# Kernel optimization log

Hardware: AMD Instinct MI355X
Metric: run time of the kernel (lower is better)

## Reference

```python
import jax, jax.numpy as jnp
from jax import lax
import numpy as np

NDIM = 256
BATCH = 65536
NROT = NDIM * (NDIM - 1) // 2  # comb(ndim, 2) = 32640


def _givens_mat(rots, ii, jj, ndim):
    """Product G_last @ ... @ G_1 of Givens rotations in combinations order.

    Left-multiplying by G(i, j, theta) only modifies rows i and j, so we apply
    each rotation as a rank-2 row update instead of a full matmul (same math
    as the original `plane_rot_mat @ mat` loop).
    """
    def step(mat, carry):
        i, j, th = carry
        c = jnp.cos(th)
        s = jnp.sin(th)
        ri = mat[i]
        rj = mat[j]
        mat = mat.at[i].set(c * ri - s * rj)
        mat = mat.at[j].set(s * ri + c * rj)
        return mat, None

    mat0 = jnp.eye(ndim, dtype=jnp.complex64)
    mat, _ = lax.scan(step, mat0, (ii, jj, rots))
    return mat


def setup_inputs() -> dict:
    key = jax.random.key(0)
    k1, k2, k3, k4 = jax.random.split(key, 4)
    x = jax.random.normal(k1, (BATCH, NDIM), dtype=jnp.float32)
    rots1 = 0.1 * jax.random.normal(k2, (NROT,), dtype=jnp.float32)
    phases = 0.1 * jax.random.normal(k3, (NDIM,), dtype=jnp.float32)
    rots2 = 0.1 * jax.random.normal(k4, (NROT,), dtype=jnp.float32)
    return {"x": x, "rots1": rots1, "phases": phases, "rots2": rots2}


def reference(x, rots1, phases, rots2):
    ndim = x.shape[1]
    # np.triu_indices(ndim, 1) enumerates (i, j) pairs in the same row-major
    # order as itertools.combinations(range(ndim), 2).
    ii_np, jj_np = np.triu_indices(ndim, k=1)
    ii = jnp.asarray(ii_np, dtype=jnp.int32)
    jj = jnp.asarray(jj_np, dtype=jnp.int32)

    # vector_norm: row-wise L2 normalization
    xn = x / jnp.linalg.norm(x, axis=1, keepdims=True)
    xc = xn.astype(jnp.complex64)

    # rot1: y = x @ M1.T with M1 = G_last @ ... @ G_1
    M1 = _givens_mat(rots1, ii, jj, ndim)
    y = xc @ M1.T

    # phase_transforms: x @ diag(exp(i*phases)) == elementwise phase multiply
    y = y * jnp.exp(1j * phases)

    # rot2
    M2 = _givens_mat(rots2, ii, jj, ndim)
    y = y @ M2.T

    # measure: |.|^2
    return jnp.abs(y) ** 2
```

## Files before the change

### kernel.cpp

```cpp
#include <hip/hip_runtime.h>
#include <stdint.h>
#include <math.h>

#define NDIM 256
#define BATCH 65536
#define NROT 32640

typedef float  f32x4 __attribute__((ext_vector_type(4)));
typedef short  s16x8 __attribute__((ext_vector_type(8)));
typedef unsigned int u32x4 __attribute__((ext_vector_type(4)));
typedef unsigned int u32x2 __attribute__((ext_vector_type(2)));

static __device__ __forceinline__ unsigned short f2bf(float f) {
    unsigned int u = __float_as_uint(f);
    u += 0x7fffu + ((u >> 16) & 1u);
    return (unsigned short)(u >> 16);
}
static __device__ __forceinline__ float bf2f(unsigned short h) {
    return __uint_as_float(((unsigned)h) << 16);
}

static __device__ __forceinline__ void split4(f32x4 v, u32x2* hi, u32x2* lo) {
    unsigned short h[4], l[4];
    #pragma unroll
    for (int i = 0; i < 4; i++) {
        h[i] = f2bf(v[i]);
        l[i] = f2bf(v[i] - bf2f(h[i]));
    }
    *hi = (u32x2){ (unsigned)h[0] | ((unsigned)h[1] << 16),
                   (unsigned)h[2] | ((unsigned)h[3] << 16) };
    *lo = (u32x2){ (unsigned)l[0] | ((unsigned)l[1] << 16),
                   (unsigned)l[2] | ((unsigned)l[3] << 16) };
}
static __device__ __forceinline__ void split8(const float* v, u32x4* hi, u32x4* lo) {
    unsigned short h[8], l[8];
    #pragma unroll
    for (int i = 0; i < 8; i++) {
        h[i] = f2bf(v[i]);
        l[i] = f2bf(v[i] - bf2f(h[i]));
    }
    *hi = (u32x4){ (unsigned)h[0] | ((unsigned)h[1] << 16),
                   (unsigned)h[2] | ((unsigned)h[3] << 16),
                   (unsigned)h[4] | ((unsigned)h[5] << 16),
                   (unsigned)h[6] | ((unsigned)h[7] << 16) };
    *lo = (u32x4){ (unsigned)l[0] | ((unsigned)l[1] << 16),
                   (unsigned)l[2] | ((unsigned)l[3] << 16),
                   (unsigned)l[4] | ((unsigned)l[5] << 16),
                   (unsigned)l[6] | ((unsigned)l[7] << 16) };
}

static __device__ __forceinline__ int sweep_bound(int k, int pblk) {
    int target = k * (NROT / pblk);
    int best = 0, bd = 0x7fffffff;
    for (int i = 0; i <= 256; i += 4) {
        int pre = i * 255 - (i * (i - 1)) / 2;
        int d = pre - target; d = (d < 0) ? -d : d;
        if (d < bd) { bd = d; best = i; }
    }
    return best;
}

__global__ __launch_bounds__(256) void k_cs(const float* __restrict__ r1,
                                            const float* __restrict__ r2,
                                            float2* __restrict__ cs) {
    int i = blockIdx.x * 256 + threadIdx.x;
    float th = (i < NROT) ? r1[i] : r2[i - NROT];
    float sv, cv; sincosf(th, &sv, &cv);
    cs[i] = make_float2(cv, sv);
}

__global__ __launch_bounds__(64) void k_blocks(const float2* __restrict__ cs,
                                               float* __restrict__ bmats, int pblk) {
    __shared__ float colb[264 * 64];
    __shared__ float2 csb[2][256 * 4];
    __shared__ float2 tri[24 * 6];

    const int t = threadIdx.x;
    const int bid = blockIdx.x;
    const int chunk = bid & 3;
    const int b = (bid >> 2) % pblk;
    const int set = (bid >> 2) / pblk;
    const int col0 = chunk * 64;
    const float2* cst = cs + (size_t)set * NROT;

    const int s0 = sweep_bound(b, pblk);
    const int s1 = sweep_bound(b + 1, pblk);
    const int ngroups = (s1 - s0) >> 2;

    {
        const f32x4 z = {0.f, 0.f, 0.f, 0.f};
        #pragma unroll 11
        for (int q = 0; q < 66; q++)
            *(f32x4*)&colb[(q * 64 + t) * 4] = z;
        colb[(col0 + t) * 64 + t] = 1.0f;
    }

    for (int k = t; k < ngroups * 6; k += 64) {
        int g = k / 6, q = k - g * 6;
        int a  = (q < 3) ? 0 : ((q < 5) ? 1 : 2);
        int bb = (q < 3) ? (q + 1) : ((q < 5) ? (q - 1) : 3);
        int m0 = s0 + g * 4;
        int m = m0 + a;
        int base = m * 255 - (m * (m - 1)) / 2;
        tri[k] = cst[base - m - 1 + m0 + bb];
    }

    float2 gv[16];
    {
        const int m0g = s0;
        int offg[4];
        #pragma unroll
        for (int a = 0; a < 4; a++) {
            int m = m0g + a;
            offg[a] = m * 255 - (m * (m - 1)) / 2 - m - 1;
        }
        #pragma unroll
        for (int it = 0; it < 16; it++) {
            int k = t + it * 64;
            int jj = k >> 2, a = k & 3;
            int j = m0g + 4 + jj;
            gv[it] = (j < 256) ? cst[offg[a] + j] : make_float2(1.f, 0.f);
        }
        #pragma unroll
        for (int it = 0; it < 16; it++)
            csb[0][t + it * 64] = gv[it];
    }

    for (int g = 0; g < ngroups; g++) {
        const int m0 = s0 + g * 4;
        const int buf = g & 1;
        const int n_j = 252 - m0;
        const int n_p = (n_j > 0) ? ((n_j + 7) & ~7) : 0;
        const float* csbuf = (const float*)&csb[buf][0];

        const bool have_next = (g + 1 < ngroups);
        if (have_next) {
            const int m0g = m0 + 4;
            int offg[4];
            #pragma unroll
            for (int a = 0; a < 4; a++) {
                int m = m0g + a;
                offg[a] = m * 255 - (m * (m - 1)) / 2 - m - 1;
            }
            #pragma unroll
            for (int it = 0; it < 16; it++) {
                int k = t + it * 64;
                int jj = k >> 2, a = k & 3;
                int j = m0g + 4 + jj;
                gv[it] = (j < 256) ? cst[offg[a] + j] : make_float2(1.f, 0.f);
            }
        }

        float u0 = colb[(m0 + 0) * 64 + t];
        float u1 = colb[(m0 + 1) * 64 + t];
        float u2 = colb[(m0 + 2) * 64 + t];
        float u3 = colb[(m0 + 3) * 64 + t];

        {
            float2 cv; float nr;
            cv = tri[g * 6 + 0]; nr = cv.y * u0 + cv.x * u1; u0 = cv.x * u0 - cv.y * u1; u1 = nr;
            cv = tri[g * 6 + 1]; nr = cv.y * u0 + cv.x * u2; u0 = cv.x * u0 - cv.y * u2; u2 = nr;
            cv = tri[g * 6 + 2]; nr = cv.y * u0 + cv.x * u3; u0 = cv.x * u0 - cv.y * u3; u3 = nr;
            cv = tri[g * 6 + 3]; nr = cv.y * u1 + cv.x * u2; u1 = cv.x * u1 - cv.y * u2; u2 = nr;
            cv = tri[g * 6 + 4]; nr = cv.y * u1 + cv.x * u3; u1 = cv.x * u1 - cv.y * u3; u3 = nr;
            cv = tri[g * 6 + 5]; nr = cv.y * u2 + cv.x * u3; u2 = cv.x * u2 - cv.y * u3; u3 = nr;
        }

        if (n_p > 0) {
            float rbuf[8];
            f32x4 abuf[8][2];
            #pragma unroll
            for (int p = 0; p < 8; p++) {
                rbuf[p] = colb[(m0 + 4 + p) * 64 + t];
                abuf[p][0] = *(const f32x4*)&csbuf[p * 8 + 0];
                abuf[p][1] = *(const f32x4*)&csbuf[p * 8 + 4];
            }
            for (int c = 0; c < n_p; c += 8) {
                #pragma unroll
                for (int p = 0; p < 8; p++) {
                    const int j = m0 + 4 + c + p;
                    float r = rbuf[p];
                    f32x4 A01 = abuf[p][0], A23 = abuf[p][1];
                    int jn = j + 8; jn = (jn < 263) ? jn : 263;
                    int cn = c + p + 8; cn = (cn < n_p) ? cn : (n_p - 1);
                    rbuf[p] = colb[jn * 64 + t];
                    abuf[p][0] = *(const f32x4*)&csbuf[cn * 8 + 0];
                    abuf[p][1] = *(const f32x4*)&csbuf[cn * 8 + 4];
                    float nr;
                    nr = A01[1] * u0 + A01[0] * r; u0 = A01[0] * u0 - A01[1] * r; r = nr;
                    nr = A01[3] * u1 + A01[2] * r; u1 = A01[2] * u1 - A01[3] * r; r = nr;
                    nr = A23[1] * u2 + A23[0] * r; u2 = A23[0] * u2 - A23[1] * r; r = nr;
                    nr = A23[3] * u3 + A23[2] * r; u3 = A23[2] * u3 - A23[3] * r; r = nr;
                    colb[j * 64 + t] = r;
                }
            }
        }
        colb[(m0 + 0) * 64 + t] = u0;
        colb[(m0 + 1) * 64 + t] = u1;
        colb[(m0 + 2) * 64 + t] = u2;
        colb[(m0 + 3) * 64 + t] = u3;

        if (have_next) {
            #pragma unroll
            for (int it = 0; it < 16; it++)
                csb[buf ^ 1][t + it * 64] = gv[it];
        }
    }

    float* outm = bmats + (size_t)(set * pblk + b) * 65536;
    for (int r = 0; r < 256; r++)
        outm[(size_t)r * 256 + col0 + t] = colb[r * 64 + t];
}

__global__ __launch_bounds__(256) void k_combine(const float* __restrict__ src,
                                                 float* __restrict__ dst,
                                                 int half, int pblk,
                                                 const float* __restrict__ xg,
                                                 unsigned short* __restrict__ xbf) {
    const int by = blockIdx.y;
    const int tid = threadIdx.x;

    if (by >= 2 * half) {
        const int id = (by - 2 * half) * 16 + blockIdx.x;
        const int w = tid >> 6, lane = tid & 63;
        const int r0 = id * 64;
        #pragma unroll 2
        for (int p = 0; p < 16; p++) {
            int row = r0 + p * 4 + w;
            f32x4 v = *(const f32x4*)&xg[(size_t)row * 256 + lane * 4];
            float s = v[0] * v[0] + v[1] * v[1] + v[2] * v[2] + v[3] * v[3];
            #pragma unroll
            for (int off = 32; off; off >>= 1) s += __shfl_xor(s, off, 64);
            float sc = 1.0f / sqrtf(s);
            unsigned short h0 = f2bf(v[0] * sc), h1 = f2bf(v[1] * sc);
            unsigned short h2 = f2bf(v[2] * sc), h3 = f2bf(v[3] * sc);
            u32x2 pk = { (unsigned)h0 | ((unsigned)h1 << 16),
                         (unsigned)h2 | ((unsigned)h3 << 16) };
            *(u32x2*)&xbf[(size_t)row * 256 + lane * 4] = pk;
        }
        return;
    }

    const int set = by / half, pidx = by % half;
    const int stride = pblk / (2 * half);
    const int s0A = sweep_bound((2 * pidx + 1) * stride, pblk);
    const float* Am = src + (size_t)(set * 2 * half + 2 * pidx + 1) * 65536;
    const float* Bm = src + (size_t)(set * 2 * half + 2 * pidx) * 65536;
    float* Dm = dst + (size_t)(set * half + pidx) * 65536;
    const int tr = blockIdx.x >> 2, tc = blockIdx.x & 3;

    if (tr * 64 + 64 <= s0A) {
        #pragma unroll
        for (int it = 0; it < 4; it++) {
            int flat = tid + it * 256;
            int r = flat >> 4, c4 = flat & 15;
            size_t idx = (size_t)(tr * 64 + r) * 256 + tc * 64 + c4 * 4;
            *(f32x4*)&Dm[idx] = *(const f32x4*)&Bm[idx];
        }
        return;
    }
    const int kb0 = (tr * 64 >= s0A) ? (s0A >> 5) : 0;

    __shared__ unsigned short Ahi[64 * 40], Alo[64 * 40];
    __shared__ unsigned short Bhi[64 * 40], Blo[64 * 40];

    const int lane = tid & 63, w = tid >> 6;
    const int mh = (w >> 1) * 32, nh = (w & 1) * 32;
    const int l15 = lane & 15, lq = lane >> 4;
    const int bn = tid & 63, bkq = tid >> 6;

    f32x4 acc[2][2];
    #pragma unroll
    for (int i = 0; i < 2; i++)
        #pragma unroll
        for (int j = 0; j < 2; j++) acc[i][j] = (f32x4){0.f, 0.f, 0.f, 0.f};

    for (int kb = kb0; kb < 8; kb++) {
        __syncthreads();
        #pragma unroll
        for (int it = 0; it < 2; it++) {
            int flat = tid + it * 256;
            int r = flat >> 3, c4 = flat & 7;
            f32x4 v = *(const f32x4*)&Am[(size_t)(tr * 64 + r) * 256 + kb * 32 + c4 * 4];
            u32x2 hi, lo; split4(v, &hi, &lo);
            *(u32x2*)&Ahi[r * 40 + c4 * 4] = hi;
            *(u32x2*)&Alo[r * 40 + c4 * 4] = lo;
        }
        {
            float bv[8];
            #pragma unroll
            for (int i = 0; i < 8; i++)
                bv[i] = Bm[(size_t)(kb * 32 + bkq * 8 + i) * 256 + tc * 64 + bn];
            u32x4 hi, lo; split8(bv, &hi, &lo);
            *(u32x4*)&Bhi[bn * 40 + bkq * 8] = hi;
            *(u32x4*)&Blo[bn * 40 + bkq * 8] = lo;
        }
        __syncthreads();
        s16x8 ah[2], al[2], bh[2], bl[2];
        #pragma unroll
        for (int tm = 0; tm < 2; tm++) {
            ah[tm] = *(const s16x8*)&Ahi[(mh + tm * 16 + l15) * 40 + lq * 8];
            al[tm] = *(const s16x8*)&Alo[(mh + tm * 16 + l15) * 40 + lq * 8];
        }
        #pragma unroll
        for (int tn = 0; tn < 2; tn++) {
            bh[tn] = *(const s16x8*)&Bhi[(nh + tn * 16 + l15) * 40 + lq * 8];
            bl[tn] = *(const s16x8*)&Blo[(nh + tn * 16 + l15) * 40 + lq * 8];
        }
        #pragma unroll
        for (int tm = 0; tm < 2; tm++)
            #pragma unroll
            for (int tn = 0; tn < 2; tn++) {
                acc[tm][tn] = __builtin_amdgcn_mfma_f32_16x16x32_bf16(ah[tm], bh[tn], acc[tm][tn], 0, 0, 0);
                acc[tm][tn] = __builtin_amdgcn_mfma_f32_16x16x32_bf16(ah[tm], bl[tn], acc[tm][tn], 0, 0, 0);
                acc[tm][tn] = __builtin_amdgcn_mfma_f32_16x16x32_bf16(al[tm], bh[tn], acc[tm][tn], 0, 0, 0);
            }
    }
    #pragma unroll
    for (int tm = 0; tm < 2; tm++)
        #pragma unroll
        for (int tn = 0; tn < 2; tn++)
            #pragma unroll
            for (int r = 0; r < 4; r++)
                Dm[(size_t)(tr * 64 + mh + tm * 16 + lq * 4 + r) * 256
                   + tc * 64 + nh + tn * 16 + l15] = acc[tm][tn][r];
}

__global__ __launch_bounds__(256) void k_abt(const float* __restrict__ mats,
                                             const float* __restrict__ phases,
                                             unsigned short* __restrict__ abt) {
    const float* Am = mats + 65536;
    const float* Bm = mats;
    const int v = blockIdx.y;
    const int tr = blockIdx.x >> 2, tc = blockIdx.x & 3;
    const int tid = threadIdx.x;

    __shared__ unsigned short Ahi[64 * 40], Alo[64 * 40];
    __shared__ unsigned short Bhi[64 * 40], Blo[64 * 40];

    const int lane = tid & 63, w = tid >> 6;
    const int mh = (w >> 1) * 32, nh = (w & 1) * 32;
    const int l15 = lane & 15, lq = lane >> 4;
    const int bn = tid & 63, bkq = tid >> 6;

    f32x4 acc[2][2];
    #pragma unroll
    for (int i = 0; i < 2; i++)
        #pragma unroll
        for (int j = 0; j < 2; j++) acc[i][j] = (f32x4){0.f, 0.f, 0.f, 0.f};

    for (int kb = 0; kb < 8; kb++) {
        __syncthreads();
        #pragma unroll
        for (int it = 0; it < 2; it++) {
            int flat = tid + it * 256;
            int r = flat >> 3, c4 = flat & 7;
            f32x4 vv = *(const f32x4*)&Am[(size_t)(tr * 64 + r) * 256 + kb * 32 + c4 * 4];
            u32x2 hi, lo; split4(vv, &hi, &lo);
            *(u32x2*)&Ahi[r * 40 + c4 * 4] = hi;
            *(u32x2*)&Alo[r * 40 + c4 * 4] = lo;
        }
        {
            float bv[8];
            #pragma unroll
            for (int i = 0; i < 8; i++) {
                int kg = kb * 32 + bkq * 8 + i;
                float ph = phases[kg];
                float sc = v ? sinf(ph) : cosf(ph);
                bv[i] = Bm[(size_t)kg * 256 + tc * 64 + bn] * sc;
            }
            u32x4 hi, lo; split8(bv, &hi, &lo);
            *(u32x4*)&Bhi[bn * 40 + bkq * 8] = hi;
            *(u32x4*)&Blo[bn * 40 + bkq * 8] = lo;
        }
        __syncthreads();
        s16x8 ah[2], al[2], bh[2], bl[2];
        #pragma unroll
        for (int tm = 0; tm < 2; tm++) {
            ah[tm] = *(const s16x8*)&Ahi[(mh + tm * 16 + l15) * 40 + lq * 8];
            al[tm] = *(const s16x8*)&Alo[(mh + tm * 16 + l15) * 40 + lq * 8];
        }
        #pragma unroll
        for (int tn = 0; tn < 2; tn++) {
            bh[tn] = *(const s16x8*)&Bhi[(nh + tn * 16 + l15) * 40 + lq * 8];
            bl[tn] = *(const s16x8*)&Blo[(nh + tn * 16 + l15) * 40 + lq * 8];
        }
        #pragma unroll
        for (int tm = 0; tm < 2; tm++)
            #pragma unroll
            for (int tn = 0; tn < 2; tn++) {
                acc[tm][tn] = __builtin_amdgcn_mfma_f32_16x16x32_bf16(ah[tm], bh[tn], acc[tm][tn], 0, 0, 0);
                acc[tm][tn] = __builtin_amdgcn_mfma_f32_16x16x32_bf16(ah[tm], bl[tn], acc[tm][tn], 0, 0, 0);
                acc[tm][tn] = __builtin_amdgcn_mfma_f32_16x16x32_bf16(al[tm], bh[tn], acc[tm][tn], 0, 0, 0);
            }
    }
    #pragma unroll
    for (int tm = 0; tm < 2; tm++)
        #pragma unroll
        for (int tn = 0; tn < 2; tn++)
            #pragma unroll
            for (int r = 0; r < 4; r++)
                abt[(size_t)(v * 256 + tr * 64 + mh + tm * 16 + lq * 4 + r) * 256
                    + tc * 64 + nh + tn * 16 + l15] = f2bf(acc[tm][tn][r]);
}

__global__ __launch_bounds__(256) void k_norm(const float* __restrict__ x,
                                              float* __restrict__ invn) {
    const int row = blockIdx.x * 4 + (threadIdx.x >> 6);
    const int lane = threadIdx.x & 63;
    f32x4 v = *(const f32x4*)&x[(size_t)row * 256 + lane * 4];
    float s = v[0] * v[0] + v[1] * v[1] + v[2] * v[2] + v[3] * v[3];
    for (int off = 32; off; off >>= 1) s += __shfl_xor(s, off, 64);
    if (lane == 0) invn[row] = 1.0f / sqrtf(s);
}

#define BKP 136
__global__ __launch_bounds__(256) void k_gemm_bf(const unsigned short* __restrict__ xbf,
                                                 const unsigned short* __restrict__ abt,
                                                 float* __restrict__ out) {
    __shared__ unsigned short As[128 * BKP];
    __shared__ unsigned short Bs[128 * BKP];
    const int tid = threadIdx.x;
    const int l  = blockIdx.y * 4 + blockIdx.x;
    const int L  = (l & 7) * 256 + (l >> 3);
    const int cb = L & 3;
    const int rb = L >> 2;
    const int lane = tid & 63, w = tid >> 6;

    f32x4 acc[16];
    #pragma unroll
    for (int i = 0; i < 16; i++) acc[i] = (f32x4){0.f, 0.f, 0.f, 0.f};

    int rA[8], cA[8], grB[8];
    #pragma unroll
    for (int it = 0; it < 8; it++) {
        int flat = tid + it * 256;
        rA[it] = flat >> 4; cA[it] = flat & 15;
        int r = rA[it];
        grB[it] = (r < 64) ? (cb * 64 + r) : (256 + cb * 64 + (r - 64));
    }

    u32x4 pa[8], pb[8];
    #pragma unroll
    for (int it = 0; it < 8; it++) {
        pa[it] = *(const u32x4*)&xbf[(size_t)(rb * 128 + rA[it]) * 256 + cA[it] * 8];
        pb[it] = *(const u32x4*)&abt[(size_t)grB[it] * 256 + cA[it] * 8];
    }
    #pragma unroll
    for (int it = 0; it < 8; it++) {
        *(u32x4*)&As[rA[it] * BKP + cA[it] * 8] = pa[it];
        *(u32x4*)&Bs[rA[it] * BKP + cA[it] * 8] = pb[it];
    }
    __syncthreads();
    #pragma unroll
    for (int it = 0; it < 8; it++) {
        pa[it] = *(const u32x4*)&xbf[(size_t)(rb * 128 + rA[it]) * 256 + 128 + cA[it] * 8];
        pb[it] = *(const u32x4*)&abt[(size_t)grB[it] * 256 + 128 + cA[it] * 8];
    }

    auto compute = [&]() {
        #pragma unroll
        for (int ks = 0; ks < 4; ks++) {
            const int k0 = ks * 32 + (lane >> 4) * 8;
            s16x8 a[2], b[8];
            #pragma unroll
            for (int tm = 0; tm < 2; tm++)
                a[tm] = *(const s16x8*)&As[(w * 32 + tm * 16 + (lane & 15)) * BKP + k0];
            #pragma unroll
            for (int tn = 0; tn < 8; tn++)
                b[tn] = *(const s16x8*)&Bs[(tn * 16 + (lane & 15)) * BKP + k0];
            #pragma unroll
            for (int tm = 0; tm < 2; tm++)
                #pragma unroll
                for (int tn = 0; tn < 8; tn++)
                    acc[tm * 8 + tn] = __builtin_amdgcn_mfma_f32_16x16x32_bf16(
                        a[tm], b[tn], acc[tm * 8 + tn], 0, 0, 0);
        }
    };
    compute();
    __syncthreads();
    #pragma unroll
    for (int it = 0; it < 8; it++) {
        *(u32x4*)&As[rA[it] * BKP + cA[it] * 8] = pa[it];
        *(u32x4*)&Bs[rA[it] * BKP + cA[it] * 8] = pb[it];
    }
    __syncthreads();
    compute();

    const int qr = lane >> 4, c = lane & 15;
    #pragma unroll
    for (int tm = 0; tm < 2; tm++) {
        #pragma unroll
        for (int tn = 0; tn < 4; tn++) {
            f32x4 p = acc[tm * 8 + tn];
            f32x4 q = acc[tm * 8 + tn + 4];
            #pragma unroll
            for (int r = 0; r < 4; r++) {
                int m = w * 32 + tm * 16 + qr * 4 + r;
                out[(size_t)(rb * 128 + m) * 256 + cb * 64 + tn * 16 + c] =
                    p[r] * p[r] + q[r] * q[r];
            }
        }
    }
}

__global__ __launch_bounds__(256) void k_gemm_f32(const float* __restrict__ x,
                                                  const unsigned short* __restrict__ abt,
                                                  const float* __restrict__ invn,
                                                  float* __restrict__ out) {
    __shared__ unsigned short As[128 * BKP];
    __shared__ unsigned short Bs[128 * BKP];
    const int tid = threadIdx.x;
    const int l  = blockIdx.y * 4 + blockIdx.x;
    const int L  = (l & 7) * 256 + (l >> 3);
    const int cb = L & 3;
    const int rb = L >> 2;
    const int lane = tid & 63, w = tid >> 6;

    f32x4 acc[16];
    #pragma unroll
    for (int i = 0; i < 16; i++) acc[i] = (f32x4){0.f, 0.f, 0.f, 0.f};

    for (int kb = 0; kb < 2; kb++) {
        __syncthreads();
        #pragma unroll
        for (int it = 0; it < 16; it++) {
            int flat = tid + it * 256;
            int r = flat >> 5, c4 = flat & 31;
            f32x4 v = *(const f32x4*)&x[(size_t)(rb * 128 + r) * 256 + kb * 128 + c4 * 4];
            float sc = invn[rb * 128 + r];
            v[0] *= sc; v[1] *= sc; v[2] *= sc; v[3] *= sc;
            unsigned short h0 = f2bf(v[0]), h1 = f2bf(v[1]);
            unsigned short h2 = f2bf(v[2]), h3 = f2bf(v[3]);
            u32x2 pk = { (unsigned)h0 | ((unsigned)h1 << 16),
                         (unsigned)h2 | ((unsigned)h3 << 16) };
            *(u32x2*)&As[r * BKP + c4 * 4] = pk;
        }
        #pragma unroll
        for (int it = 0; it < 8; it++) {
            int flat = tid + it * 256;
            int r = flat >> 4, c8 = flat & 15;
            int gr = (r < 64) ? (cb * 64 + r) : (256 + cb * 64 + (r - 64));
            u32x4 vv = *(const u32x4*)&abt[(size_t)gr * 256 + kb * 128 + c8 * 8];
            *(u32x4*)&Bs[r * BKP + c8 * 8] = vv;
        }
        __syncthreads();
        #pragma unroll
        for (int ks = 0; ks < 4; ks++) {
            const int k0 = ks * 32 + (lane >> 4) * 8;
            s16x8 a[2], b[8];
            #pragma unroll
            for (int tm = 0; tm < 2; tm++)
                a[tm] = *(const s16x8*)&As[(w * 32 + tm * 16 + (lane & 15)) * BKP + k0];
            #pragma unroll
            for (int tn = 0; tn < 8; tn++)
                b[tn] = *(const s16x8*)&Bs[(tn * 16 + (lane & 15)) * BKP + k0];
            #pragma unroll
            for (int tm = 0; tm < 2; tm++)
                #pragma unroll
                for (int tn = 0; tn < 8; tn++)
                    acc[tm * 8 + tn] = __builtin_amdgcn_mfma_f32_16x16x32_bf16(
                        a[tm], b[tn], acc[tm * 8 + tn], 0, 0, 0);
        }
    }

    const int qr = lane >> 4, c = lane & 15;
    #pragma unroll
    for (int tm = 0; tm < 2; tm++) {
        #pragma unroll
        for (int tn = 0; tn < 4; tn++) {
            f32x4 p = acc[tm * 8 + tn];
            f32x4 q = acc[tm * 8 + tn + 4];
            #pragma unroll
            for (int r = 0; r < 4; r++) {
                int m = w * 32 + tm * 16 + qr * 4 + r;
                out[(size_t)(rb * 128 + m) * 256 + cb * 64 + tn * 16 + c] =
                    p[r] * p[r] + q[r] * q[r];
            }
        }
    }
}

extern "C" void kernel_launch(void* const* d_in, const int* in_sizes, int n_in,
                              void* d_out, int out_size, void* d_ws, size_t ws_size,
                              hipStream_t stream) {
    (void)in_sizes; (void)n_in; (void)out_size;
    const float* x      = (const float*)d_in[0];
    const float* rots1  = (const float*)d_in[1];
    const float* phases = (const float*)d_in[2];
    const float* rots2  = (const float*)d_in[3];
    float* out = (float*)d_out;
    char* ws = (char*)d_ws;

    const size_t MAT = 262144;
    int pblk = 32;
    while (pblk > 16 &&
           (size_t)3 * pblk * MAT + 2 * MAT + (size_t)BATCH * 512 > ws_size)
        pblk >>= 1;
    const size_t offA   = 0;
    const size_t offB   = offA + (size_t)2 * pblk * MAT;
    const size_t offABT = offB + (size_t)pblk * MAT;
    const size_t offINV = offABT + MAT;
    const size_t offXBF = offINV + MAT;
    const bool use_xbf = (offXBF + (size_t)BATCH * 512) <= ws_size;

    float*          A    = (float*)(ws + offA);
    float*          B    = (float*)(ws + offB);
    unsigned short* abt  = (unsigned short*)(ws + offABT);
    float*          invn = (float*)(ws + offINV);
    unsigned short* xbf  = (unsigned short*)(ws + offXBF);
    float2*         cs   = (float2*)(ws + offB);

    k_cs<<<(2 * NROT) / 256, 256, 0, stream>>>(rots1, rots2, cs);
    k_blocks<<<8 * pblk, 64, 0, stream>>>(cs, A, pblk);

    float* srcp = A; float* dstp = B;
    bool first = true;
    for (int half = pblk / 2; half >= 1; half >>= 1) {
        const int xny = (first && use_xbf) ? 64 : 0;
        k_combine<<<dim3(16, 2 * half + xny), 256, 0, stream>>>(srcp, dstp, half, pblk,
                                                                x, xbf);
        float* tmp = srcp; srcp = dstp; dstp = tmp;
        first = false;
    }
    k_abt<<<dim3(16, 2), 256, 0, stream>>>(srcp, phases, abt);

    if (use_xbf) {
        k_gemm_bf<<<dim3(4, BATCH / 128), 256, 0, stream>>>(xbf, abt, out);
    } else {
        k_norm<<<BATCH / 4, 256, 0, stream>>>(x, invn);
        k_gemm_f32<<<dim3(4, BATCH / 128), 256, 0, stream>>>(x, abt, invn, out);
    }
}
```

Before: 263.4 us.

## Fuse combine tree and abt into one cooperative kernel; inline sincos into k_blocks

Replaces the sequence of per-level k_combine launches plus k_abt with a single cooperative persistent kernel that uses grid-wide syncs between tree levels, and folds the x normalisation work into the first level. It also removes the separate k_cs kernel by computing sincos directly inside k_blocks. This aims to cut kernel launch gaps and tail idle time across the many small launches. The costs are grid.sync overhead, redundant sincos evaluation across the column-chunk blocks, and reliance on cooperative launch support, with the old path kept as a fallback.

```diff
diff --git a/kernel.cpp b/kernel.cpp
--- a/kernel.cpp
+++ b/kernel.cpp
@@ -1,4 +1,5 @@
 #include <hip/hip_runtime.h>
+#include <hip/hip_cooperative_groups.h>
 #include <stdint.h>
 #include <math.h>
 
@@ -60,16 +61,8 @@
     return best;
 }
 
-__global__ __launch_bounds__(256) void k_cs(const float* __restrict__ r1,
-                                            const float* __restrict__ r2,
-                                            float2* __restrict__ cs) {
-    int i = blockIdx.x * 256 + threadIdx.x;
-    float th = (i < NROT) ? r1[i] : r2[i - NROT];
-    float sv, cv; sincosf(th, &sv, &cv);
-    cs[i] = make_float2(cv, sv);
-}
-
-__global__ __launch_bounds__(64) void k_blocks(const float2* __restrict__ cs,
+__global__ __launch_bounds__(64) void k_blocks(const float* __restrict__ r1,
+                                               const float* __restrict__ r2,
                                                float* __restrict__ bmats, int pblk) {
     __shared__ float colb[264 * 64];
     __shared__ float2 csb[2][256 * 4];
@@ -81,7 +74,7 @@
     const int b = (bid >> 2) % pblk;
     const int set = (bid >> 2) / pblk;
     const int col0 = chunk * 64;
-    const float2* cst = cs + (size_t)set * NROT;
+    const float* rots = set ? r2 : r1;
 
     const int s0 = sweep_bound(b, pblk);
     const int s1 = sweep_bound(b + 1, pblk);
@@ -102,7 +95,9 @@
         int m0 = s0 + g * 4;
         int m = m0 + a;
         int base = m * 255 - (m * (m - 1)) / 2;
-        tri[k] = cst[base - m - 1 + m0 + bb];
+        float th = rots[base - m - 1 + m0 + bb];
+        float sv, cv; sincosf(th, &sv, &cv);
+        tri[k] = make_float2(cv, sv);
     }
 
     float2 gv[16];
@@ -119,7 +114,10 @@
             int k = t + it * 64;
             int jj = k >> 2, a = k & 3;
             int j = m0g + 4 + jj;
-            gv[it] = (j < 256) ? cst[offg[a] + j] : make_float2(1.f, 0.f);
+            if (j < 256) {
+                float sv, cv; sincosf(rots[offg[a] + j], &sv, &cv);
+                gv[it] = make_float2(cv, sv);
+            } else gv[it] = make_float2(1.f, 0.f);
         }
         #pragma unroll
         for (int it = 0; it < 16; it++)
@@ -147,7 +145,10 @@
                 int k = t + it * 64;
                 int jj = k >> 2, a = k & 3;
                 int j = m0g + 4 + jj;
-                gv[it] = (j < 256) ? cst[offg[a] + j] : make_float2(1.f, 0.f);
+                if (j < 256) {
+                    float sv, cv; sincosf(rots[offg[a] + j], &sv, &cv);
+                    gv[it] = make_float2(cv, sv);
+                } else gv[it] = make_float2(1.f, 0.f);
             }
         }
 
@@ -212,42 +213,40 @@
         outm[(size_t)r * 256 + col0 + t] = colb[r * 64 + t];
 }
 
-__global__ __launch_bounds__(256) void k_combine(const float* __restrict__ src,
-                                                 float* __restrict__ dst,
-                                                 int half, int pblk,
-                                                 const float* __restrict__ xg,
-                                                 unsigned short* __restrict__ xbf) {
-    const int by = blockIdx.y;
-    const int tid = threadIdx.x;
-
-    if (by >= 2 * half) {
-        const int id = (by - 2 * half) * 16 + blockIdx.x;
-        const int w = tid >> 6, lane = tid & 63;
-        const int r0 = id * 64;
-        #pragma unroll 2
-        for (int p = 0; p < 16; p++) {
-            int row = r0 + p * 4 + w;
-            f32x4 v = *(const f32x4*)&xg[(size_t)row * 256 + lane * 4];
-            float s = v[0] * v[0] + v[1] * v[1] + v[2] * v[2] + v[3] * v[3];
-            #pragma unroll
-            for (int off = 32; off; off >>= 1) s += __shfl_xor(s, off, 64);
-            float sc = 1.0f / sqrtf(s);
-            unsigned short h0 = f2bf(v[0] * sc), h1 = f2bf(v[1] * sc);
-            unsigned short h2 = f2bf(v[2] * sc), h3 = f2bf(v[3] * sc);
-            u32x2 pk = { (unsigned)h0 | ((unsigned)h1 << 16),
-                         (unsigned)h2 | ((unsigned)h3 << 16) };
-            *(u32x2*)&xbf[(size_t)row * 256 + lane * 4] = pk;
-        }
-        return;
-    }
-
+
+static __device__ __forceinline__ void xnorm_item(const float* __restrict__ xg,
+                                                  unsigned short* __restrict__ xbf,
+                                                  int id, int tid) {
+    const int w = tid >> 6, lane = tid & 63;
+    const int r0 = id * 64;
+    #pragma unroll 2
+    for (int p = 0; p < 16; p++) {
+        int row = r0 + p * 4 + w;
+        f32x4 v = *(const f32x4*)&xg[(size_t)row * 256 + lane * 4];
+        float s = v[0] * v[0] + v[1] * v[1] + v[2] * v[2] + v[3] * v[3];
+        #pragma unroll
+        for (int off = 32; off; off >>= 1) s += __shfl_xor(s, off, 64);
+        float sc = 1.0f / sqrtf(s);
+        unsigned short h0 = f2bf(v[0] * sc), h1 = f2bf(v[1] * sc);
+        unsigned short h2 = f2bf(v[2] * sc), h3 = f2bf(v[3] * sc);
+        u32x2 pk = { (unsigned)h0 | ((unsigned)h1 << 16),
+                     (unsigned)h2 | ((unsigned)h3 << 16) };
+        *(u32x2*)&xbf[(size_t)row * 256 + lane * 4] = pk;
+    }
+}
+
+static __device__ void combine_tile(const float* __restrict__ src,
+                                    float* __restrict__ dst,
+                                    int half, int pblk, int bx, int by, int tid,
+                                    unsigned short* Ahi, unsigned short* Alo,
+                                    unsigned short* Bhi, unsigned short* Blo) {
     const int set = by / half, pidx = by % half;
     const int stride = pblk / (2 * half);
     const int s0A = sweep_bound((2 * pidx + 1) * stride, pblk);
     const float* Am = src + (size_t)(set * 2 * half + 2 * pidx + 1) * 65536;
     const float* Bm = src + (size_t)(set * 2 * half + 2 * pidx) * 65536;
     float* Dm = dst + (size_t)(set * half + pidx) * 65536;
-    const int tr = blockIdx.x >> 2, tc = blockIdx.x & 3;
+    const int tr = bx >> 2, tc = bx & 3;
 
     if (tr * 64 + 64 <= s0A) {
         #pragma unroll
@@ -260,9 +259,6 @@
         return;
     }
     const int kb0 = (tr * 64 >= s0A) ? (s0A >> 5) : 0;
-
-    __shared__ unsigned short Ahi[64 * 40], Alo[64 * 40];
-    __shared__ unsigned short Bhi[64 * 40], Blo[64 * 40];
 
     const int lane = tid & 63, w = tid >> 6;
     const int mh = (w >> 1) * 32, nh = (w & 1) * 32;
@@ -326,17 +322,15 @@
                    + tc * 64 + nh + tn * 16 + l15] = acc[tm][tn][r];
 }
 
-__global__ __launch_bounds__(256) void k_abt(const float* __restrict__ mats,
-                                             const float* __restrict__ phases,
-                                             unsigned short* __restrict__ abt) {
+static __device__ void abt_tile(const float* __restrict__ mats,
+                                const float* __restrict__ phases,
+                                unsigned short* __restrict__ abtp,
+                                int bx, int v, int tid,
+                                unsigned short* Ahi, unsigned short* Alo,
+                                unsigned short* Bhi, unsigned short* Blo) {
     const float* Am = mats + 65536;
     const float* Bm = mats;
-    const int v = blockIdx.y;
-    const int tr = blockIdx.x >> 2, tc = blockIdx.x & 3;
-    const int tid = threadIdx.x;
-
-    __shared__ unsigned short Ahi[64 * 40], Alo[64 * 40];
-    __shared__ unsigned short Bhi[64 * 40], Blo[64 * 40];
+    const int tr = bx >> 2, tc = bx & 3;
 
     const int lane = tid & 63, w = tid >> 6;
     const int mh = (w >> 1) * 32, nh = (w & 1) * 32;
@@ -400,8 +394,66 @@
         for (int tn = 0; tn < 2; tn++)
             #pragma unroll
             for (int r = 0; r < 4; r++)
-                abt[(size_t)(v * 256 + tr * 64 + mh + tm * 16 + lq * 4 + r) * 256
-                    + tc * 64 + nh + tn * 16 + l15] = f2bf(acc[tm][tn][r]);
+                abtp[(size_t)(v * 256 + tr * 64 + mh + tm * 16 + lq * 4 + r) * 256
+                     + tc * 64 + nh + tn * 16 + l15] = f2bf(acc[tm][tn][r]);
+}
+
+__global__ __launch_bounds__(256) void k_tree(const float* __restrict__ A0,
+                                              float* __restrict__ B0,
+                                              int pblk,
+                                              const float* __restrict__ phases,
+                                              unsigned short* __restrict__ abtp,
+                                              const float* __restrict__ xg,
+                                              unsigned short* __restrict__ xbf,
+                                              int do_xn) {
+    __shared__ unsigned short Ahi[64 * 40], Alo[64 * 40];
+    __shared__ unsigned short Bhi[64 * 40], Blo[64 * 40];
+    cooperative_groups::grid_group grid = cooperative_groups::this_grid();
+    const int GW = gridDim.x;
+    const int tid = threadIdx.x;
+    const float* srcp = A0;
+    float* dstp = B0;
+    int first = 1;
+    for (int half = pblk / 2; half >= 1; half >>= 1) {
+        const int ctiles = 16 * 2 * half;
+        const int items = ctiles + ((first && do_xn) ? 1024 : 0);
+        for (int it = blockIdx.x; it < items; it += GW) {
+            if (it < ctiles)
+                combine_tile(srcp, dstp, half, pblk, it & 15, it >> 4, tid,
+                             Ahi, Alo, Bhi, Blo);
+            else
+                xnorm_item(xg, xbf, it - ctiles, tid);
+        }
+        grid.sync();
+        const float* ts = srcp; srcp = dstp; dstp = (float*)ts;
+        first = 0;
+    }
+    for (int it = blockIdx.x; it < 32; it += GW)
+        abt_tile(srcp, phases, abtp, it & 15, it >> 4, tid, Ahi, Alo, Bhi, Blo);
+}
+
+__global__ __launch_bounds__(256) void k_combine(const float* __restrict__ src,
+                                                 float* __restrict__ dst,
+                                                 int half, int pblk,
+                                                 const float* __restrict__ xg,
+                                                 unsigned short* __restrict__ xbf) {
+    __shared__ unsigned short Ahi[64 * 40], Alo[64 * 40];
+    __shared__ unsigned short Bhi[64 * 40], Blo[64 * 40];
+    const int by = blockIdx.y, tid = threadIdx.x;
+    if (by >= 2 * half) {
+        xnorm_item(xg, xbf, (by - 2 * half) * 16 + blockIdx.x, tid);
+        return;
+    }
+    combine_tile(src, dst, half, pblk, blockIdx.x, by, tid, Ahi, Alo, Bhi, Blo);
+}
+
+__global__ __launch_bounds__(256) void k_abt(const float* __restrict__ mats,
+                                             const float* __restrict__ phases,
+                                             unsigned short* __restrict__ abtp) {
+    __shared__ unsigned short Ahi[64 * 40], Alo[64 * 40];
+    __shared__ unsigned short Bhi[64 * 40], Blo[64 * 40];
+    abt_tile(mats, phases, abtp, blockIdx.x, blockIdx.y, threadIdx.x,
+             Ahi, Alo, Bhi, Blo);
 }
 
 __global__ __launch_bounds__(256) void k_norm(const float* __restrict__ x,
@@ -609,21 +661,35 @@
     unsigned short* abt  = (unsigned short*)(ws + offABT);
     float*          invn = (float*)(ws + offINV);
     unsigned short* xbf  = (unsigned short*)(ws + offXBF);
-    float2*         cs   = (float2*)(ws + offB);
-
-    k_cs<<<(2 * NROT) / 256, 256, 0, stream>>>(rots1, rots2, cs);
-    k_blocks<<<8 * pblk, 64, 0, stream>>>(cs, A, pblk);
-
-    float* srcp = A; float* dstp = B;
-    bool first = true;
-    for (int half = pblk / 2; half >= 1; half >>= 1) {
-        const int xny = (first && use_xbf) ? 64 : 0;
-        k_combine<<<dim3(16, 2 * half + xny), 256, 0, stream>>>(srcp, dstp, half, pblk,
-                                                                x, xbf);
-        float* tmp = srcp; srcp = dstp; dstp = tmp;
-        first = false;
-    }
-    k_abt<<<dim3(16, 2), 256, 0, stream>>>(srcp, phases, abt);
+
+    k_blocks<<<8 * pblk, 64, 0, stream>>>(rots1, rots2, A, pblk);
+
+    bool coop_ok = false;
+    if (use_xbf) {
+        int maxb = 0;
+        if (hipOccupancyMaxActiveBlocksPerMultiprocessor(&maxb, k_tree, 256, 0)
+                == hipSuccess && maxb >= 1) {
+            int gw = maxb * 256; if (gw > 1024) gw = 1024;
+            int do_xn = 1;
+            void* kargs[] = { (void*)&A, (void*)&B, (void*)&pblk, (void*)&phases,
+                              (void*)&abt, (void*)&x, (void*)&xbf, (void*)&do_xn };
+            if (hipLaunchCooperativeKernel((void*)k_tree, dim3(gw), dim3(256),
+                                           kargs, 0, stream) == hipSuccess)
+                coop_ok = true;
+        }
+    }
+    if (!coop_ok) {
+        float* srcp = A; float* dstp = B;
+        bool first = true;
+        for (int half = pblk / 2; half >= 1; half >>= 1) {
+            const int xny = (first && use_xbf) ? 64 : 0;
+            k_combine<<<dim3(16, 2 * half + xny), 256, 0, stream>>>(srcp, dstp, half,
+                                                                    pblk, x, xbf);
+            float* tmp = srcp; srcp = dstp; dstp = tmp;
+            first = false;
+        }
+        k_abt<<<dim3(16, 2), 256, 0, stream>>>(srcp, phases, abt);
+    }
 
     if (use_xbf) {
         k_gemm_bf<<<dim3(4, BATCH / 128), 256, 0, stream>>>(xbf, abt, out);
```

New measurement: 438.1 us. +66.3%, slower.

## Double-buffer shared tiles and prefetch two k-steps ahead in combine and abt kernels

Applied to the files above, without the earlier changes.

Restructures the split-bf16 MFMA tile loops in k_combine and k_abt into a register-prefetched, double-buffered LDS pipeline. Global loads for tile k+2 are issued while tile k+1 is split into shared memory and tile k is multiplied, which leaves one barrier per step instead of two. The aim is to hide global-load latency in these small, latency-bound matrix-combine kernels. In exchange it doubles LDS use per block (about 40 KB) and raises register pressure, which could lower occupancy. The final large GEMM is unchanged.

```diff
diff --git a/kernel.cpp b/kernel.cpp
--- a/kernel.cpp
+++ b/kernel.cpp
@@ -212,42 +212,103 @@
         outm[(size_t)r * 256 + col0 + t] = colb[r * 64 + t];
 }
 
-__global__ __launch_bounds__(256) void k_combine(const float* __restrict__ src,
-                                                 float* __restrict__ dst,
-                                                 int half, int pblk,
-                                                 const float* __restrict__ xg,
-                                                 unsigned short* __restrict__ xbf) {
-    const int by = blockIdx.y;
-    const int tid = threadIdx.x;
-
-    if (by >= 2 * half) {
-        const int id = (by - 2 * half) * 16 + blockIdx.x;
-        const int w = tid >> 6, lane = tid & 63;
-        const int r0 = id * 64;
-        #pragma unroll 2
-        for (int p = 0; p < 16; p++) {
-            int row = r0 + p * 4 + w;
-            f32x4 v = *(const f32x4*)&xg[(size_t)row * 256 + lane * 4];
-            float s = v[0] * v[0] + v[1] * v[1] + v[2] * v[2] + v[3] * v[3];
-            #pragma unroll
-            for (int off = 32; off; off >>= 1) s += __shfl_xor(s, off, 64);
-            float sc = 1.0f / sqrtf(s);
-            unsigned short h0 = f2bf(v[0] * sc), h1 = f2bf(v[1] * sc);
-            unsigned short h2 = f2bf(v[2] * sc), h3 = f2bf(v[3] * sc);
-            u32x2 pk = { (unsigned)h0 | ((unsigned)h1 << 16),
-                         (unsigned)h2 | ((unsigned)h3 << 16) };
-            *(u32x2*)&xbf[(size_t)row * 256 + lane * 4] = pk;
-        }
-        return;
-    }
-
+static __device__ __forceinline__ void xnorm_item(const float* __restrict__ xg,
+                                                  unsigned short* __restrict__ xbf,
+                                                  int id, int tid) {
+    const int w = tid >> 6, lane = tid & 63;
+    const int r0 = id * 64;
+    #pragma unroll 2
+    for (int p = 0; p < 16; p++) {
+        int row = r0 + p * 4 + w;
+        f32x4 v = *(const f32x4*)&xg[(size_t)row * 256 + lane * 4];
+        float s = v[0] * v[0] + v[1] * v[1] + v[2] * v[2] + v[3] * v[3];
+        #pragma unroll
+        for (int off = 32; off; off >>= 1) s += __shfl_xor(s, off, 64);
+        float sc = 1.0f / sqrtf(s);
+        unsigned short h0 = f2bf(v[0] * sc), h1 = f2bf(v[1] * sc);
+        unsigned short h2 = f2bf(v[2] * sc), h3 = f2bf(v[3] * sc);
+        u32x2 pk = { (unsigned)h0 | ((unsigned)h1 << 16),
+                     (unsigned)h2 | ((unsigned)h3 << 16) };
+        *(u32x2*)&xbf[(size_t)row * 256 + lane * 4] = pk;
+    }
+}
+
+#define TB 2560
+
+static __device__ __forceinline__ void tile_issueA(const float* __restrict__ Am,
+                                                   int tr, int kb, int tid,
+                                                   f32x4 va[2]) {
+    #pragma unroll
+    for (int it = 0; it < 2; it++) {
+        int flat = tid + it * 256;
+        int r = flat >> 3, c4 = flat & 7;
+        va[it] = *(const f32x4*)&Am[(size_t)(tr * 64 + r) * 256 + kb * 32 + c4 * 4];
+    }
+}
+static __device__ __forceinline__ void tile_issueB(const float* __restrict__ Bm,
+                                                   int tc, int kb, int bn, int bkq,
+                                                   float vb[8]) {
+    #pragma unroll
+    for (int i = 0; i < 8; i++)
+        vb[i] = Bm[(size_t)(kb * 32 + bkq * 8 + i) * 256 + tc * 64 + bn];
+}
+static __device__ __forceinline__ void tile_commit(unsigned short* __restrict__ Ahi,
+                                                   unsigned short* __restrict__ Alo,
+                                                   unsigned short* __restrict__ Bhi,
+                                                   unsigned short* __restrict__ Blo,
+                                                   int tid, int bn, int bkq,
+                                                   const f32x4 va[2], const float vb[8]) {
+    #pragma unroll
+    for (int it = 0; it < 2; it++) {
+        int flat = tid + it * 256;
+        int r = flat >> 3, c4 = flat & 7;
+        u32x2 hi, lo; split4(va[it], &hi, &lo);
+        *(u32x2*)&Ahi[r * 40 + c4 * 4] = hi;
+        *(u32x2*)&Alo[r * 40 + c4 * 4] = lo;
+    }
+    u32x4 hi8, lo8; split8(vb, &hi8, &lo8);
+    *(u32x4*)&Bhi[bn * 40 + bkq * 8] = hi8;
+    *(u32x4*)&Blo[bn * 40 + bkq * 8] = lo8;
+}
+static __device__ __forceinline__ void tile_mfma(const unsigned short* __restrict__ Ahi,
+                                                 const unsigned short* __restrict__ Alo,
+                                                 const unsigned short* __restrict__ Bhi,
+                                                 const unsigned short* __restrict__ Blo,
+                                                 int mh, int nh, int l15, int lq,
+                                                 f32x4 acc[2][2]) {
+    s16x8 ah[2], al[2], bh[2], bl[2];
+    #pragma unroll
+    for (int tm = 0; tm < 2; tm++) {
+        ah[tm] = *(const s16x8*)&Ahi[(mh + tm * 16 + l15) * 40 + lq * 8];
+        al[tm] = *(const s16x8*)&Alo[(mh + tm * 16 + l15) * 40 + lq * 8];
+    }
+    #pragma unroll
+    for (int tn = 0; tn < 2; tn++) {
+        bh[tn] = *(const s16x8*)&Bhi[(nh + tn * 16 + l15) * 40 + lq * 8];
+        bl[tn] = *(const s16x8*)&Blo[(nh + tn * 16 + l15) * 40 + lq * 8];
+    }
+    #pragma unroll
+    for (int tm = 0; tm < 2; tm++)
+        #pragma unroll
+        for (int tn = 0; tn < 2; tn++) {
+            acc[tm][tn] = __builtin_amdgcn_mfma_f32_16x16x32_bf16(ah[tm], bh[tn], acc[tm][tn], 0, 0, 0);
+            acc[tm][tn] = __builtin_amdgcn_mfma_f32_16x16x32_bf16(ah[tm], bl[tn], acc[tm][tn], 0, 0, 0);
+            acc[tm][tn] = __builtin_amdgcn_mfma_f32_16x16x32_bf16(al[tm], bh[tn], acc[tm][tn], 0, 0, 0);
+        }
+}
+
+static __device__ void combine_tile(const float* __restrict__ src,
+                                    float* __restrict__ dst,
+                                    int half, int pblk, int bx, int by, int tid,
+                                    unsigned short* Ahi, unsigned short* Alo,
+                                    unsigned short* Bhi, unsigned short* Blo) {
     const int set = by / half, pidx = by % half;
     const int stride = pblk / (2 * half);
     const int s0A = sweep_bound((2 * pidx + 1) * stride, pblk);
     const float* Am = src + (size_t)(set * 2 * half + 2 * pidx + 1) * 65536;
     const float* Bm = src + (size_t)(set * 2 * half + 2 * pidx) * 65536;
     float* Dm = dst + (size_t)(set * half + pidx) * 65536;
-    const int tr = blockIdx.x >> 2, tc = blockIdx.x & 3;
+    const int tr = bx >> 2, tc = bx & 3;
 
     if (tr * 64 + 64 <= s0A) {
         #pragma unroll
@@ -261,9 +322,6 @@
     }
     const int kb0 = (tr * 64 >= s0A) ? (s0A >> 5) : 0;
 
-    __shared__ unsigned short Ahi[64 * 40], Alo[64 * 40];
-    __shared__ unsigned short Bhi[64 * 40], Blo[64 * 40];
-
     const int lane = tid & 63, w = tid >> 6;
     const int mh = (w >> 1) * 32, nh = (w & 1) * 32;
     const int l15 = lane & 15, lq = lane >> 4;
@@ -275,46 +333,37 @@
         #pragma unroll
         for (int j = 0; j < 2; j++) acc[i][j] = (f32x4){0.f, 0.f, 0.f, 0.f};
 
+    f32x4 vaE[2], vaO[2]; float vbE[8], vbO[8];
+    tile_issueA(Am, tr, kb0, tid, vaE);
+    tile_issueB(Bm, tc, kb0, bn, bkq, vbE);
+    if (kb0 + 1 < 8) {
+        tile_issueA(Am, tr, kb0 + 1, tid, vaO);
+        tile_issueB(Bm, tc, kb0 + 1, bn, bkq, vbO);
+    }
+    tile_commit(Ahi, Alo, Bhi, Blo, tid, bn, bkq, vaE, vbE);
+    __syncthreads();
+
     for (int kb = kb0; kb < 8; kb++) {
+        const int cur = (kb - kb0) & 1;
+        if (cur == 0) {
+            if (kb + 2 < 8) {
+                tile_issueA(Am, tr, kb + 2, tid, vaE);
+                tile_issueB(Bm, tc, kb + 2, bn, bkq, vbE);
+            }
+            if (kb + 1 < 8)
+                tile_commit(Ahi + TB, Alo + TB, Bhi + TB, Blo + TB,
+                            tid, bn, bkq, vaO, vbO);
+            tile_mfma(Ahi, Alo, Bhi, Blo, mh, nh, l15, lq, acc);
+        } else {
+            if (kb + 2 < 8) {
+                tile_issueA(Am, tr, kb + 2, tid, vaO);
+                tile_issueB(Bm, tc, kb + 2, bn, bkq, vbO);
+            }
+            if (kb + 1 < 8)
+                tile_commit(Ahi, Alo, Bhi, Blo, tid, bn, bkq, vaE, vbE);
+            tile_mfma(Ahi + TB, Alo + TB, Bhi + TB, Blo + TB, mh, nh, l15, lq, acc);
+        }
         __syncthreads();
-        #pragma unroll
-        for (int it = 0; it < 2; it++) {
-            int flat = tid + it * 256;
-            int r = flat >> 3, c4 = flat & 7;
-            f32x4 v = *(const f32x4*)&Am[(size_t)(tr * 64 + r) * 256 + kb * 32 + c4 * 4];
-            u32x2 hi, lo; split4(v, &hi, &lo);
-            *(u32x2*)&Ahi[r * 40 + c4 * 4] = hi;
-            *(u32x2*)&Alo[r * 40 + c4 * 4] = lo;
-        }
-        {
-            float bv[8];
-            #pragma unroll
-            for (int i = 0; i < 8; i++)
-                bv[i] = Bm[(size_t)(kb * 32 + bkq * 8 + i) * 256 + tc * 64 + bn];
-            u32x4 hi, lo; split8(bv, &hi, &lo);
-            *(u32x4*)&Bhi[bn * 40 + bkq * 8] = hi;
-            *(u32x4*)&Blo[bn * 40 + bkq * 8] = lo;
-        }
-        __syncthreads();
-        s16x8 ah[2], al[2], bh[2], bl[2];
-        #pragma unroll
-        for (int tm = 0; tm < 2; tm++) {
-            ah[tm] = *(const s16x8*)&Ahi[(mh + tm * 16 + l15) * 40 + lq * 8];
-            al[tm] = *(const s16x8*)&Alo[(mh + tm * 16 + l15) * 40 + lq * 8];
-        }
-        #pragma unroll
-        for (int tn = 0; tn < 2; tn++) {
-            bh[tn] = *(const s16x8*)&Bhi[(nh + tn * 16 + l15) * 40 + lq * 8];
-            bl[tn] = *(const s16x8*)&Blo[(nh + tn * 16 + l15) * 40 + lq * 8];
-        }
-        #pragma unroll
-        for (int tm = 0; tm < 2; tm++)
-            #pragma unroll
-            for (int tn = 0; tn < 2; tn++) {
-                acc[tm][tn] = __builtin_amdgcn_mfma_f32_16x16x32_bf16(ah[tm], bh[tn], acc[tm][tn], 0, 0, 0);
-                acc[tm][tn] = __builtin_amdgcn_mfma_f32_16x16x32_bf16(ah[tm], bl[tn], acc[tm][tn], 0, 0, 0);
-                acc[tm][tn] = __builtin_amdgcn_mfma_f32_16x16x32_bf16(al[tm], bh[tn], acc[tm][tn], 0, 0, 0);
-            }
     }
     #pragma unroll
     for (int tm = 0; tm < 2; tm++)
@@ -326,17 +375,15 @@
                    + tc * 64 + nh + tn * 16 + l15] = acc[tm][tn][r];
 }
 
-__global__ __launch_bounds__(256) void k_abt(const float* __restrict__ mats,
-                                             const float* __restrict__ phases,
-                                             unsigned short* __restrict__ abt) {
+static __device__ void abt_tile(const float* __restrict__ mats,
+                                const float* __restrict__ phases,
+                                unsigned short* __restrict__ abtp,
+                                int bx, int v, int tid,
+                                unsigned short* Ahi, unsigned short* Alo,
+                                unsigned short* Bhi, unsigned short* Blo) {
     const float* Am = mats + 65536;
     const float* Bm = mats;
-    const int v = blockIdx.y;
-    const int tr = blockIdx.x >> 2, tc = blockIdx.x & 3;
-    const int tid = threadIdx.x;
-
-    __shared__ unsigned short Ahi[64 * 40], Alo[64 * 40];
-    __shared__ unsigned short Bhi[64 * 40], Blo[64 * 40];
+    const int tr = bx >> 2, tc = bx & 3;
 
     const int lane = tid & 63, w = tid >> 6;
     const int mh = (w >> 1) * 32, nh = (w & 1) * 32;
@@ -349,50 +396,37 @@
         #pragma unroll
         for (int j = 0; j < 2; j++) acc[i][j] = (f32x4){0.f, 0.f, 0.f, 0.f};
 
+    auto issueBs = [&](int kb, float vb[8]) {
+        #pragma unroll
+        for (int i = 0; i < 8; i++) {
+            int kg = kb * 32 + bkq * 8 + i;
+            float ph = phases[kg];
+            float sc = v ? sinf(ph) : cosf(ph);
+            vb[i] = Bm[(size_t)kg * 256 + tc * 64 + bn] * sc;
+        }
+    };
+
+    f32x4 vaE[2], vaO[2]; float vbE[8], vbO[8];
+    tile_issueA(Am, tr, 0, tid, vaE); issueBs(0, vbE);
+    tile_issueA(Am, tr, 1, tid, vaO); issueBs(1, vbO);
+    tile_commit(Ahi, Alo, Bhi, Blo, tid, bn, bkq, vaE, vbE);
+    __syncthreads();
+
     for (int kb = 0; kb < 8; kb++) {
+        const int cur = kb & 1;
+        if (cur == 0) {
+            if (kb + 2 < 8) { tile_issueA(Am, tr, kb + 2, tid, vaE); issueBs(kb + 2, vbE); }
+            if (kb + 1 < 8)
+                tile_commit(Ahi + TB, Alo + TB, Bhi + TB, Blo + TB,
+                            tid, bn, bkq, vaO, vbO);
+            tile_mfma(Ahi, Alo, Bhi, Blo, mh, nh, l15, lq, acc);
+        } else {
+            if (kb + 2 < 8) { tile_issueA(Am, tr, kb + 2, tid, vaO); issueBs(kb + 2, vbO); }
+            if (kb + 1 < 8)
+                tile_commit(Ahi, Alo, Bhi, Blo, tid, bn, bkq, vaE, vbE);
+            tile_mfma(Ahi + TB, Alo + TB, Bhi + TB, Blo + TB, mh, nh, l15, lq, acc);
+        }
         __syncthreads();
-        #pragma unroll
-        for (int it = 0; it < 2; it++) {
-            int flat = tid + it * 256;
-            int r = flat >> 3, c4 = flat & 7;
-            f32x4 vv = *(const f32x4*)&Am[(size_t)(tr * 64 + r) * 256 + kb * 32 + c4 * 4];
-            u32x2 hi, lo; split4(vv, &hi, &lo);
-            *(u32x2*)&Ahi[r * 40 + c4 * 4] = hi;
-            *(u32x2*)&Alo[r * 40 + c4 * 4] = lo;
-        }
-        {
-            float bv[8];
-            #pragma unroll
-            for (int i = 0; i < 8; i++) {
-                int kg = kb * 32 + bkq * 8 + i;
-                float ph = phases[kg];
-                float sc = v ? sinf(ph) : cosf(ph);
-                bv[i] = Bm[(size_t)kg * 256 + tc * 64 + bn] * sc;
-            }
-            u32x4 hi, lo; split8(bv, &hi, &lo);
-            *(u32x4*)&Bhi[bn * 40 + bkq * 8] = hi;
-            *(u32x4*)&Blo[bn * 40 + bkq * 8] = lo;
-        }
-        __syncthreads();
-        s16x8 ah[2], al[2], bh[2], bl[2];
-        #pragma unroll
-        for (int tm = 0; tm < 2; tm++) {
-            ah[tm] = *(const s16x8*)&Ahi[(mh + tm * 16 + l15) * 40 + lq * 8];
-            al[tm] = *(const s16x8*)&Alo[(mh + tm * 16 + l15) * 40 + lq * 8];
-        }
-        #pragma unroll
-        for (int tn = 0; tn < 2; tn++) {
-            bh[tn] = *(const s16x8*)&Bhi[(nh + tn * 16 + l15) * 40 + lq * 8];
-            bl[tn] = *(const s16x8*)&Blo[(nh + tn * 16 + l15) * 40 + lq * 8];
-        }
-        #pragma unroll
-        for (int tm = 0; tm < 2; tm++)
-            #pragma unroll
-            for (int tn = 0; tn < 2; tn++) {
-                acc[tm][tn] = __builtin_amdgcn_mfma_f32_16x16x32_bf16(ah[tm], bh[tn], acc[tm][tn], 0, 0, 0);
-                acc[tm][tn] = __builtin_amdgcn_mfma_f32_16x16x32_bf16(ah[tm], bl[tn], acc[tm][tn], 0, 0, 0);
-                acc[tm][tn] = __builtin_amdgcn_mfma_f32_16x16x32_bf16(al[tm], bh[tn], acc[tm][tn], 0, 0, 0);
-            }
     }
     #pragma unroll
     for (int tm = 0; tm < 2; tm++)
@@ -400,8 +434,30 @@
         for (int tn = 0; tn < 2; tn++)
             #pragma unroll
             for (int r = 0; r < 4; r++)
-                abt[(size_t)(v * 256 + tr * 64 + mh + tm * 16 + lq * 4 + r) * 256
-                    + tc * 64 + nh + tn * 16 + l15] = f2bf(acc[tm][tn][r]);
+                abtp[(size_t)(v * 256 + tr * 64 + mh + tm * 16 + lq * 4 + r) * 256
+                     + tc * 64 + nh + tn * 16 + l15] = f2bf(acc[tm][tn][r]);
+}
+
+__global__ __launch_bounds__(256) void k_combine(const float* __restrict__ src,
+                                                 float* __restrict__ dst,
+                                                 int half, int pblk,
+                                                 const float* __restrict__ xg,
+                                                 unsigned short* __restrict__ xbf) {
+    __shared__ unsigned short Ahi[2 * TB], Alo[2 * TB], Bhi[2 * TB], Blo[2 * TB];
+    const int by = blockIdx.y, tid = threadIdx.x;
+    if (by >= 2 * half) {
+        xnorm_item(xg, xbf, (by - 2 * half) * 16 + blockIdx.x, tid);
+        return;
+    }
+    combine_tile(src, dst, half, pblk, blockIdx.x, by, tid, Ahi, Alo, Bhi, Blo);
+}
+
+__global__ __launch_bounds__(256) void k_abt(const float* __restrict__ mats,
+                                             const float* __restrict__ phases,
+                                             unsigned short* __restrict__ abtp) {
+    __shared__ unsigned short Ahi[2 * TB], Alo[2 * TB], Bhi[2 * TB], Blo[2 * TB];
+    abt_tile(mats, phases, abtp, blockIdx.x, blockIdx.y, threadIdx.x,
+             Ahi, Alo, Bhi, Blo);
 }
 
 __global__ __launch_bounds__(256) void k_norm(const float* __restrict__ x,
@@ -618,8 +674,8 @@
     bool first = true;
     for (int half = pblk / 2; half >= 1; half >>= 1) {
         const int xny = (first && use_xbf) ? 64 : 0;
-        k_combine<<<dim3(16, 2 * half + xny), 256, 0, stream>>>(srcp, dstp, half, pblk,
-                                                                x, xbf);
+        k_combine<<<dim3(16, 2 * half + xny), 256, 0, stream>>>(srcp, dstp, half,
+                                                                pblk, x, xbf);
         float* tmp = srcp; srcp = dstp; dstp = tmp;
         first = false;
     }
```

Result: no change. 267.3 us (+1.5%).
